# Performance work log

Measured on AMD Instinct MI355X. Metric: run time of the kernel, lower is better.

## Reference

```python
import jax, jax.numpy as jnp
import numpy as np
from jax import lax

# Resolved Optuna hyperparameters
NPOINTS = (512, 256, 128)
RADII = (0.2, 0.4, 0.8)
KS = (32, 32, 32)
BN_EPS = 1e-5


def _fps_single(pts, npoint):
    """Farthest point sampling on one cloud. pts: (N,3) -> (npoint,) int32."""
    N = pts.shape[0]
    def step(carry, _):
        dists, last = carry
        d = jnp.sum((pts - pts[last]) ** 2, axis=-1)
        dists = jnp.minimum(dists, d)
        nxt = jnp.argmax(dists).astype(jnp.int32)
        return (dists, nxt), last
    init = (jnp.full((N,), 1e10, pts.dtype), jnp.int32(0))
    (_, _), idx = lax.scan(step, init, None, length=npoint)
    return idx


def _set_abstraction(xyz, feat, W, b, radius, k, npoint):
    """xyz: (B,N,3), feat: (B,N,C_in) -> new_xyz (B,S,3), new_feat (B,S,C_out)."""
    B, N, _ = xyz.shape
    fps_idx = jax.vmap(lambda p: _fps_single(p, npoint))(xyz)          # (B,S)
    new_xyz = jax.vmap(lambda x, i: x[i])(xyz, fps_idx)                # (B,S,3)
    # ball query: squared distances centers -> all points
    d2 = jnp.sum((new_xyz[:, :, None, :] - xyz[:, None, :, :]) ** 2, axis=-1)  # (B,S,N)
    valid = d2 <= radius * radius
    ar = jnp.arange(N, dtype=jnp.int32)
    gi = jnp.where(valid, ar[None, None, :], N)                        # invalid -> N
    gi = jnp.sort(gi, axis=-1)[:, :, :k]                               # first k in index order
    first = gi[:, :, :1]
    gi = jnp.where(gi == N, first, gi)                                 # pad with first valid (center itself)
    g_xyz = jax.vmap(lambda x, i: x[i])(xyz, gi)                       # (B,S,k,3)
    rel = g_xyz - new_xyz[:, :, None, :]
    g_feat = jax.vmap(lambda x, i: x[i])(feat, gi)                     # (B,S,k,C_in)
    h = jnp.concatenate([rel, g_feat], axis=-1)                        # (B,S,k,3+C_in)
    h = jax.nn.relu(jnp.einsum('bskc,co->bsko', h, W) + b)
    return new_xyz, jnp.max(h, axis=2)                                 # max-pool over group


def _bn(x, g, b):
    # nn.BatchNorm1d training-mode forward (batch statistics, biased var)
    m = x.mean(axis=0)
    v = x.var(axis=0)
    return (x - m) * lax.rsqrt(v + BN_EPS) * g + b


def setup_inputs() -> dict:
    key = jax.random.key(0)
    ks = jax.random.split(key, 8)
    def w(k, i, o):
        return (jax.random.normal(k, (i, o), jnp.float32) / np.sqrt(i)).astype(jnp.float32)
    return dict(
        points=jax.random.uniform(ks[0], (16, 4096, 3), jnp.float32),
        W1=w(ks[1], 3 + 3, 64),   b1=jnp.zeros((64,), jnp.float32),
        W2=w(ks[2], 64 + 3, 128), b2=jnp.zeros((128,), jnp.float32),
        W3=w(ks[3], 128 + 3, 256), b3=jnp.zeros((256,), jnp.float32),
        fc1_w=w(ks[4], 256, 256), fc1_b=jnp.zeros((256,), jnp.float32),
        fc2_w=w(ks[5], 256, 128), fc2_b=jnp.zeros((128,), jnp.float32),
        fc3_w=w(ks[6], 128, 12),  fc3_b=jnp.zeros((12,), jnp.float32),
        bn1_g=jnp.ones((256,), jnp.float32), bn1_b=jnp.zeros((256,), jnp.float32),
        bn2_g=jnp.ones((128,), jnp.float32), bn2_b=jnp.zeros((128,), jnp.float32),
    )


def reference(points, W1, b1, W2, b2, W3, b3, fc1_w, fc1_b, fc2_w, fc2_b,
              fc3_w, fc3_b, bn1_g, bn1_b, bn2_g, bn2_b):
    B = points.shape[0]
    xyz, feat = points, points
    for (W, bb, r, k, s) in ((W1, b1, RADII[0], KS[0], NPOINTS[0]),
                             (W2, b2, RADII[1], KS[1], NPOINTS[1]),
                             (W3, b3, RADII[2], KS[2], NPOINTS[2])):
        xyz, feat = _set_abstraction(xyz, feat, W, bb, r, k, s)
    f = jnp.max(feat, axis=1)                                          # (B, ch3)
    x = jax.nn.relu(_bn(f @ fc1_w + fc1_b, bn1_g, bn1_b))              # dropout: eval-mode identity
    x = jax.nn.relu(_bn(x @ fc2_w + fc2_b, bn2_g, bn2_b))
    x = x @ fc3_w + fc3_b
    return x.reshape(B, 4, 3)
```

## Files before the change

### kernel.cpp

```cpp
#include <hip/hip_runtime.h>
#include <hip/hip_bf16.h>


#define B_SZ 16

template<int CTRL>
__device__ __forceinline__ float dpp_mv(float v) {
    const int i = __float_as_int(v);
    const int r = __builtin_amdgcn_update_dpp(i, i, CTRL, 0xf, 0xf, false);
    return __int_as_float(r);
}

__device__ __forceinline__ float wave_max_f32(float x) {
    float v = x;
    v = fmaxf(v, dpp_mv<0x111>(v));
    v = fmaxf(v, dpp_mv<0x112>(v));
    v = fmaxf(v, dpp_mv<0x114>(v));
    v = fmaxf(v, dpp_mv<0x118>(v));
    v = fmaxf(v, dpp_mv<0x142>(v));
    v = fmaxf(v, dpp_mv<0x143>(v));
    return __uint_as_float(__builtin_amdgcn_readlane(__float_as_uint(v), 63));
}

__device__ __forceinline__ float read_lane_f32(float v, int l) {
    return __uint_as_float(__builtin_amdgcn_readlane(__float_as_uint(v), l));
}

template<int N, int NPOINT, int BLOCK>
__global__ __launch_bounds__(BLOCK) void fps_kernel(
    const float* __restrict__ xyz,
    float* __restrict__ newxyz)
{
    constexpr int P  = N / BLOCK;
    constexpr int NW = BLOCK / 64;
    __shared__ float4 part[2][NW];
    __shared__ float  outb[NPOINT * 3];

    const int b = blockIdx.x, tid = threadIdx.x;
    const int lane = tid & 63, w = tid >> 6;
    const float* xb = xyz + (size_t)b * N * 3;

    float px[P], py[P], pz[P], dd[P];
    const int base = tid * P;
#pragma unroll
    for (int i = 0; i < P; i++) {
        px[i] = xb[(base + i) * 3 + 0];
        py[i] = xb[(base + i) * 3 + 1];
        pz[i] = xb[(base + i) * 3 + 2];
        dd[i] = 1e10f;
    }
    float lx = xb[0], ly = xb[1], lz = xb[2];
    if (tid == 0) { outb[0] = lx; outb[1] = ly; outb[2] = lz; }

    for (int s = 1; s < NPOINT; s++) {
        float bv = -1.0f, bx = 0.0f, by = 0.0f, bz = 0.0f;
#pragma unroll
        for (int i = 0; i < P; i++) {
            const float dx = px[i] - lx, dy = py[i] - ly, dz = pz[i] - lz;
            const float d2 = __fadd_rn(__fadd_rn(__fmul_rn(dx, dx), __fmul_rn(dy, dy)),
                                       __fmul_rn(dz, dz));
            const float nd = fminf(dd[i], d2);
            dd[i] = nd;
            const bool gt = nd > bv;
            bv = gt ? nd : bv;
            bx = gt ? px[i] : bx;
            by = gt ? py[i] : by;
            bz = gt ? pz[i] : bz;
        }
        const float wmax = wave_max_f32(bv);
        const unsigned long long mset = __ballot(bv == wmax);
        const int li = __ffsll(mset) - 1;
        const int buf = s & 1;
        if (lane == li) part[buf][w] = make_float4(bv, bx, by, bz);
        __syncthreads();
        float cv = -1.0f;
#pragma unroll
        for (int q = 0; q < NW; q++) {
            const float4 pq = part[buf][q];
            const bool gt = pq.x > cv;
            cv = gt ? pq.x : cv;
            lx = gt ? pq.y : lx;
            ly = gt ? pq.z : ly;
            lz = gt ? pq.w : lz;
        }
        if (tid == 0) {
            outb[s * 3 + 0] = lx; outb[s * 3 + 1] = ly; outb[s * 3 + 2] = lz;
        }
    }
    __syncthreads();
    float* o = newxyz + (size_t)b * NPOINT * 3;
    for (int t = tid; t < NPOINT * 3; t += BLOCK) o[t] = outb[t];
}

template<int N, int NPOINT>
__device__ __forceinline__ void fps_wave_body(
    const float* __restrict__ xyz,
    float* __restrict__ newxyz,
    const int b, const int lane)
{
    constexpr int P = N / 64;
    const float* xb = xyz + (size_t)b * N * 3;

    float px[P], py[P], pz[P], dd[P];
    const int base = lane * P;
#pragma unroll
    for (int i = 0; i < P; i++) {
        px[i] = xb[(base + i) * 3 + 0];
        py[i] = xb[(base + i) * 3 + 1];
        pz[i] = xb[(base + i) * 3 + 2];
        dd[i] = 1e10f;
    }
#pragma unroll
    for (int i = 0; i < P; i++) {
        asm volatile("" : "+v"(px[i]), "+v"(py[i]), "+v"(pz[i]));
    }
    float lx = xb[0], ly = xb[1], lz = xb[2];
    if (lane == 0) {
        float* o = newxyz + (size_t)b * NPOINT * 3;
        o[0] = lx; o[1] = ly; o[2] = lz;
    }

    for (int s = 1; s < NPOINT; s++) {
        float bv = -1.0f, bx = 0.0f, by = 0.0f, bz = 0.0f;
#pragma unroll
        for (int i = 0; i < P; i++) {
            const float dx = px[i] - lx, dy = py[i] - ly, dz = pz[i] - lz;
            const float d2 = __fadd_rn(__fadd_rn(__fmul_rn(dx, dx), __fmul_rn(dy, dy)),
                                       __fmul_rn(dz, dz));
            const float nd = fminf(dd[i], d2);
            dd[i] = nd;
            const bool gt = nd > bv;
            bv = gt ? nd : bv;
            bx = gt ? px[i] : bx;
            by = gt ? py[i] : by;
            bz = gt ? pz[i] : bz;
        }
        const float wmax = wave_max_f32(bv);
        const unsigned long long mset = __ballot(bv == wmax);
        const int li = __ffsll(mset) - 1;
        lx = read_lane_f32(bx, li);
        ly = read_lane_f32(by, li);
        lz = read_lane_f32(bz, li);
        if (lane == 0) {
            float* o = newxyz + ((size_t)b * NPOINT + s) * 3;
            o[0] = lx; o[1] = ly; o[2] = lz;
        }
    }
}

template<int N, int S, int CF, int COUT, int R>
__device__ __forceinline__ void sa_body(
    const float* __restrict__ xyz,
    const float* __restrict__ feat,
    const float* __restrict__ cent,
    const float* __restrict__ W,
    const float* __restrict__ bias,
    float* __restrict__ outf,
    const float r2, const int s, const int b, const int lane)
{
    constexpr int K    = 32;
    constexpr int JT   = 16;
    constexpr int CIN  = CF + 3;
    constexpr int CINP = (CIN + 3) & ~3;
    constexpr int C4   = CIN & ~3;
    __shared__ int   gi[K];
    __shared__ float h[JT * CINP];

    const float* xb = xyz  + (size_t)b * N * 3;
    const float* fb = feat + (size_t)b * N * CF;
    const float cx = cent[((size_t)b * S + s) * 3 + 0];
    const float cy = cent[((size_t)b * S + s) * 3 + 1];
    const float cz = cent[((size_t)b * S + s) * 3 + 2];

    constexpr int RND = N / 256;
    int total = 0, g0 = 0;
    for (int r0 = 0; r0 < RND; r0++) {
        if (total >= K) break;
        float xs[4], ys[4], zs[4];
#pragma unroll
        for (int c4 = 0; c4 < 4; c4++) {
            const int p = (r0 * 4 + c4) * 64 + lane;
            xs[c4] = xb[p * 3 + 0];
            ys[c4] = xb[p * 3 + 1];
            zs[c4] = xb[p * 3 + 2];
        }
#pragma unroll
        for (int c4 = 0; c4 < 4; c4++) {
            const int p = (r0 * 4 + c4) * 64 + lane;
            const float dx = xs[c4] - cx, dy = ys[c4] - cy, dz = zs[c4] - cz;
            const float d2 = __fadd_rn(__fadd_rn(__fmul_rn(dx, dx), __fmul_rn(dy, dy)),
                                       __fmul_rn(dz, dz));
            const bool v = (d2 <= r2);
            const unsigned long long bal = __ballot(v);
            if (total == 0 && bal != 0ull) g0 = (r0 * 4 + c4) * 64 + (__ffsll(bal) - 1);
            const int pos = total + __popcll(bal & ((1ull << lane) - 1ull));
            if (v && pos < K) gi[pos] = p;
            total += __popcll(bal);
        }
    }
    if (lane == 0 && total < K) {
        for (int q = total; q < K; q++) gi[q] = g0;
    }
    __syncthreads();

    float m[R];
#pragma unroll
    for (int r = 0; r < R; r++) m[r] = -1e30f;

    for (int pass = 0; pass < K / JT; pass++) {
        for (int jj = 0; jj < JT; jj++) {
            const int idx = gi[pass * JT + jj];
            for (int c = lane; c < CIN; c += 64) {
                float val;
                if (c < 3) {
                    const float cc = (c == 0) ? cx : ((c == 1) ? cy : cz);
                    val = xb[idx * 3 + c] - cc;
                } else {
                    val = fb[(size_t)idx * CF + (c - 3)];
                }
                h[jj * CINP + c] = val;
            }
        }
        __syncthreads();

        float acc[JT][R];
#pragma unroll
        for (int jj = 0; jj < JT; jj++)
#pragma unroll
            for (int r = 0; r < R; r++) acc[jj][r] = 0.0f;

        const float* wp = W + lane;
        int c = 0;
        for (; c < C4; c += 4) {
            float wv[4][R];
#pragma unroll
            for (int q = 0; q < 4; q++)
#pragma unroll
                for (int r = 0; r < R; r++)
                    wv[q][r] = wp[(size_t)(c + q) * COUT + r * 64];
#pragma unroll
            for (int jj = 0; jj < JT; jj++) {
                const float4 hv = *(const float4*)&h[jj * CINP + c];
#pragma unroll
                for (int r = 0; r < R; r++) {
                    acc[jj][r] = fmaf(hv.x, wv[0][r], acc[jj][r]);
                    acc[jj][r] = fmaf(hv.y, wv[1][r], acc[jj][r]);
                    acc[jj][r] = fmaf(hv.z, wv[2][r], acc[jj][r]);
                    acc[jj][r] = fmaf(hv.w, wv[3][r], acc[jj][r]);
                }
            }
        }
        for (; c < CIN; c++) {
            float wv[R];
#pragma unroll
            for (int r = 0; r < R; r++) wv[r] = wp[(size_t)c * COUT + r * 64];
#pragma unroll
            for (int jj = 0; jj < JT; jj++) {
                const float hv = h[jj * CINP + c];
#pragma unroll
                for (int r = 0; r < R; r++)
                    acc[jj][r] = fmaf(hv, wv[r], acc[jj][r]);
            }
        }
#pragma unroll
        for (int jj = 0; jj < JT; jj++)
#pragma unroll
            for (int r = 0; r < R; r++) m[r] = fmaxf(m[r], acc[jj][r]);
        __syncthreads();
    }

#pragma unroll
    for (int r = 0; r < R; r++) {
        const int o = r * 64 + lane;
        outf[((size_t)b * S + s) * COUT + o] = fmaxf(bias[o] + m[r], 0.0f);
    }
}

template<int N, int S, int CF, int COUT, int R>
__global__ __launch_bounds__(64) void sa_kernel(
    const float* __restrict__ xyz, const float* __restrict__ feat,
    const float* __restrict__ cent, const float* __restrict__ W,
    const float* __restrict__ bias, float* __restrict__ outf, const float r2)
{
    sa_body<N, S, CF, COUT, R>(xyz, feat, cent, W, bias, outf, r2,
                               blockIdx.x, blockIdx.y, threadIdx.x);
}

template<int NF, int NPF, int N, int S, int CF, int COUT, int R>
__global__ __launch_bounds__(64) void fused_fps_sa_kernel(
    const float* __restrict__ fxyz,
    float* __restrict__ fnew,
    const float* __restrict__ xyz, const float* __restrict__ feat,
    const float* __restrict__ cent, const float* __restrict__ W,
    const float* __restrict__ bias, float* __restrict__ outf, const float r2)
{
    if (blockIdx.x < B_SZ) {
        __builtin_amdgcn_s_setprio(3);
        fps_wave_body<NF, NPF>(fxyz, fnew, blockIdx.x, threadIdx.x);
    } else {
        const int i = blockIdx.x - B_SZ;
        sa_body<N, S, CF, COUT, R>(xyz, feat, cent, W, bias, outf, r2,
                                   i % S, i / S, threadIdx.x);
    }
}

__global__ __launch_bounds__(256) void maxpool_kernel(
    const float* __restrict__ feat,
    float* __restrict__ out)
{
    const int b = blockIdx.x, o = threadIdx.x;
    const float* fb = feat + (size_t)b * 128 * 256 + o;
    float m = fb[0];
#pragma unroll 4
    for (int s1 = 1; s1 < 128; s1++) m = fmaxf(m, fb[(size_t)s1 * 256]);
    out[b * 256 + o] = m;
}

__global__ __launch_bounds__(256) void head_kernel(
    const float* __restrict__ f,
    const float* __restrict__ fc1_w, const float* __restrict__ fc1_b,
    const float* __restrict__ fc2_w, const float* __restrict__ fc2_b,
    const float* __restrict__ fc3_w, const float* __restrict__ fc3_b,
    const float* __restrict__ bn1_g, const float* __restrict__ bn1_b,
    const float* __restrict__ bn2_g, const float* __restrict__ bn2_b,
    float* __restrict__ out)
{
    __shared__ float fl[16 * 257];
    __shared__ float x1[16 * 257];
    __shared__ float x2[16 * 129];
    const int tid = threadIdx.x;

    for (int idx = tid; idx < 16 * 256; idx += 256) {
        const int r = idx >> 8, c = idx & 255;
        fl[r * 257 + c] = f[idx];
    }
    __syncthreads();

    {
        const int r = tid >> 4, g = tid & 15;
        float acc[16];
#pragma unroll
        for (int i = 0; i < 16; i++) acc[i] = fc1_b[g * 16 + i];
        const float* wrow = fc1_w + g * 16;
        for (int c = 0; c < 256; c++) {
            const float fv = fl[r * 257 + c];
            const float4* w4 = (const float4*)(wrow + (size_t)c * 256);
#pragma unroll
            for (int q = 0; q < 4; q++) {
                const float4 wv = w4[q];
                acc[q * 4 + 0] = fmaf(fv, wv.x, acc[q * 4 + 0]);
                acc[q * 4 + 1] = fmaf(fv, wv.y, acc[q * 4 + 1]);
                acc[q * 4 + 2] = fmaf(fv, wv.z, acc[q * 4 + 2]);
                acc[q * 4 + 3] = fmaf(fv, wv.w, acc[q * 4 + 3]);
            }
        }
#pragma unroll
        for (int i = 0; i < 16; i++) x1[r * 257 + g * 16 + i] = acc[i];
    }
    __syncthreads();
    {
        const int o = tid;
        float v[16];
#pragma unroll
        for (int r = 0; r < 16; r++) v[r] = x1[r * 257 + o];
        float m = 0.0f;
#pragma unroll
        for (int r = 0; r < 16; r++) m += v[r];
        m *= (1.0f / 16.0f);
        float var = 0.0f;
#pragma unroll
        for (int r = 0; r < 16; r++) { const float d = v[r] - m; var += d * d; }
        var *= (1.0f / 16.0f);
        const float sc = bn1_g[o] / sqrtf(var + 1e-5f);
        const float sh = bn1_b[o];
#pragma unroll
        for (int r = 0; r < 16; r++)
            x1[r * 257 + o] = fmaxf((v[r] - m) * sc + sh, 0.0f);
    }
    __syncthreads();
    {
        const int r = tid >> 4, g = tid & 15;
        float acc[8];
#pragma unroll
        for (int i = 0; i < 8; i++) acc[i] = fc2_b[g * 8 + i];
        const float* wrow = fc2_w + g * 8;
        for (int c = 0; c < 256; c++) {
            const float fv = x1[r * 257 + c];
            const float4* w4 = (const float4*)(wrow + (size_t)c * 128);
#pragma unroll
            for (int q = 0; q < 2; q++) {
                const float4 wv = w4[q];
                acc[q * 4 + 0] = fmaf(fv, wv.x, acc[q * 4 + 0]);
                acc[q * 4 + 1] = fmaf(fv, wv.y, acc[q * 4 + 1]);
                acc[q * 4 + 2] = fmaf(fv, wv.z, acc[q * 4 + 2]);
                acc[q * 4 + 3] = fmaf(fv, wv.w, acc[q * 4 + 3]);
            }
        }
#pragma unroll
        for (int i = 0; i < 8; i++) x2[r * 129 + g * 8 + i] = acc[i];
    }
    __syncthreads();
    if (tid < 128) {
        const int o = tid;
        float v[16];
#pragma unroll
        for (int r = 0; r < 16; r++) v[r] = x2[r * 129 + o];
        float m = 0.0f;
#pragma unroll
        for (int r = 0; r < 16; r++) m += v[r];
        m *= (1.0f / 16.0f);
        float var = 0.0f;
#pragma unroll
        for (int r = 0; r < 16; r++) { const float d = v[r] - m; var += d * d; }
        var *= (1.0f / 16.0f);
        const float sc = bn2_g[o] / sqrtf(var + 1e-5f);
        const float sh = bn2_b[o];
#pragma unroll
        for (int r = 0; r < 16; r++)
            x2[r * 129 + o] = fmaxf((v[r] - m) * sc + sh, 0.0f);
    }
    __syncthreads();
    if (tid < 192) {
        const int r = tid / 12, j = tid - r * 12;
        float acc = fc3_b[j];
        for (int c = 0; c < 128; c++)
            acc = fmaf(x2[r * 129 + c], fc3_w[c * 12 + j], acc);
        out[r * 12 + j] = acc;
    }
}

extern "C" void kernel_launch(void* const* d_in, const int* in_sizes, int n_in,
                              void* d_out, int out_size, void* d_ws, size_t ws_size,
                              hipStream_t stream) {
    const float* points = (const float*)d_in[0];
    const float* W1     = (const float*)d_in[1];
    const float* b1     = (const float*)d_in[2];
    const float* W2     = (const float*)d_in[3];
    const float* b2     = (const float*)d_in[4];
    const float* W3     = (const float*)d_in[5];
    const float* b3     = (const float*)d_in[6];
    const float* fc1_w  = (const float*)d_in[7];
    const float* fc1_b  = (const float*)d_in[8];
    const float* fc2_w  = (const float*)d_in[9];
    const float* fc2_b  = (const float*)d_in[10];
    const float* fc3_w  = (const float*)d_in[11];
    const float* fc3_b  = (const float*)d_in[12];
    const float* bn1_g  = (const float*)d_in[13];
    const float* bn1_b  = (const float*)d_in[14];
    const float* bn2_g  = (const float*)d_in[15];
    const float* bn2_b  = (const float*)d_in[16];
    float* out = (float*)d_out;

    float* ws   = (float*)d_ws;
    float* nx1  = ws;
    float* f1   = nx1 + 24576;
    float* nx2  = f1  + 524288;
    float* f2   = nx2 + 12288;
    float* nx3  = f2  + 524288;
    float* f3   = nx3 + 6144;
    float* fmx  = f3  + 524288;

    fps_kernel<4096, 512, 512><<<B_SZ, 512, 0, stream>>>(points, nx1);
    fused_fps_sa_kernel<512, 256, 4096, 512, 3, 64, 1>
        <<<B_SZ + 512 * B_SZ, 64, 0, stream>>>(
        nx1, nx2, points, points, nx1, W1, b1, f1, (float)(0.2 * 0.2));
    fused_fps_sa_kernel<256, 128, 512, 256, 64, 128, 2>
        <<<B_SZ + 256 * B_SZ, 64, 0, stream>>>(
        nx2, nx3, nx1, f1, nx2, W2, b2, f2, (float)(0.4 * 0.4));
    sa_kernel<256, 128, 128, 256, 4><<<dim3(128, B_SZ), 64, 0, stream>>>(
        nx2, f2, nx3, W3, b3, f3, (float)(0.8 * 0.8));
    maxpool_kernel<<<B_SZ, 256, 0, stream>>>(f3, fmx);
    head_kernel<<<1, 256, 0, stream>>>(fmx, fc1_w, fc1_b, fc2_w, fc2_b,
                                       fc3_w, fc3_b, bn1_g, bn1_b, bn2_g, bn2_b,
                                       out);
}
```

Baseline: 799.2 us.

## Split first FPS into two launches, fuse SA3 maxpool via atomics, parallelize fc1

```diff
diff --git a/kernel.cpp b/kernel.cpp
--- a/kernel.cpp
+++ b/kernel.cpp
@@ -26,15 +26,17 @@
     return __uint_as_float(__builtin_amdgcn_readlane(__float_as_uint(v), l));
 }
 
-template<int N, int NPOINT, int BLOCK>
+template<int N, int NPOINT, int BLOCK, int S0, int S1, bool FIRST>
 __global__ __launch_bounds__(BLOCK) void fps_kernel(
     const float* __restrict__ xyz,
-    float* __restrict__ newxyz)
+    float* __restrict__ newxyz,
+    float* __restrict__ dstate)
 {
     constexpr int P  = N / BLOCK;
     constexpr int NW = BLOCK / 64;
+    constexpr int O0 = FIRST ? 0 : S0;
     __shared__ float4 part[2][NW];
-    __shared__ float  outb[NPOINT * 3];
+    __shared__ float  outb[(S1 - O0) * 3];
 
     const int b = blockIdx.x, tid = threadIdx.x;
     const int lane = tid & 63, w = tid >> 6;
@@ -47,12 +49,21 @@
         px[i] = xb[(base + i) * 3 + 0];
         py[i] = xb[(base + i) * 3 + 1];
         pz[i] = xb[(base + i) * 3 + 2];
-        dd[i] = 1e10f;
-    }
-    float lx = xb[0], ly = xb[1], lz = xb[2];
-    if (tid == 0) { outb[0] = lx; outb[1] = ly; outb[2] = lz; }
-
-    for (int s = 1; s < NPOINT; s++) {
+    }
+    float lx, ly, lz;
+    if (FIRST) {
+#pragma unroll
+        for (int i = 0; i < P; i++) dd[i] = 1e10f;
+        lx = xb[0]; ly = xb[1]; lz = xb[2];
+        if (tid == 0) { outb[0] = lx; outb[1] = ly; outb[2] = lz; }
+    } else {
+#pragma unroll
+        for (int i = 0; i < P; i++) dd[i] = dstate[((size_t)b * P + i) * BLOCK + tid];
+        const float* c = newxyz + ((size_t)b * NPOINT + (S0 - 1)) * 3;
+        lx = c[0]; ly = c[1]; lz = c[2];
+    }
+
+    for (int s = S0; s < S1; s++) {
         float bv = -1.0f, bx = 0.0f, by = 0.0f, bz = 0.0f;
 #pragma unroll
         for (int i = 0; i < P; i++) {
@@ -84,12 +95,18 @@
             lz = gt ? pq.w : lz;
         }
         if (tid == 0) {
-            outb[s * 3 + 0] = lx; outb[s * 3 + 1] = ly; outb[s * 3 + 2] = lz;
-        }
-    }
-    __syncthreads();
-    float* o = newxyz + (size_t)b * NPOINT * 3;
-    for (int t = tid; t < NPOINT * 3; t += BLOCK) o[t] = outb[t];
+            const int t = (s - O0) * 3;
+            outb[t + 0] = lx; outb[t + 1] = ly; outb[t + 2] = lz;
+        }
+    }
+    __syncthreads();
+    if (S1 < NPOINT) {
+#pragma unroll
+        for (int i = 0; i < P; i++)
+            dstate[((size_t)b * P + i) * BLOCK + tid] = dd[i];
+    }
+    float* o = newxyz + ((size_t)b * NPOINT + O0) * 3;
+    for (int t = tid; t < (S1 - O0) * 3; t += BLOCK) o[t] = outb[t];
 }
 
 template<int N, int NPOINT>
@@ -148,7 +165,7 @@
     }
 }
 
-template<int N, int S, int CF, int COUT, int R>
+template<int N, int S, int CF, int COUT, int R, bool AMAX>
 __device__ __forceinline__ void sa_body(
     const float* __restrict__ xyz,
     const float* __restrict__ feat,
@@ -272,18 +289,23 @@
 #pragma unroll
     for (int r = 0; r < R; r++) {
         const int o = r * 64 + lane;
-        outf[((size_t)b * S + s) * COUT + o] = fmaxf(bias[o] + m[r], 0.0f);
-    }
-}
-
-template<int N, int S, int CF, int COUT, int R>
+        const float val = fmaxf(bias[o] + m[r], 0.0f);
+        if (AMAX) {
+            atomicMax((unsigned*)&outf[(size_t)b * COUT + o], __float_as_uint(val));
+        } else {
+            outf[((size_t)b * S + s) * COUT + o] = val;
+        }
+    }
+}
+
+template<int N, int S, int CF, int COUT, int R, bool AMAX>
 __global__ __launch_bounds__(64) void sa_kernel(
     const float* __restrict__ xyz, const float* __restrict__ feat,
     const float* __restrict__ cent, const float* __restrict__ W,
     const float* __restrict__ bias, float* __restrict__ outf, const float r2)
 {
-    sa_body<N, S, CF, COUT, R>(xyz, feat, cent, W, bias, outf, r2,
-                               blockIdx.x, blockIdx.y, threadIdx.x);
+    sa_body<N, S, CF, COUT, R, AMAX>(xyz, feat, cent, W, bias, outf, r2,
+                                     blockIdx.x, blockIdx.y, threadIdx.x);
 }
 
 template<int NF, int NPF, int N, int S, int CF, int COUT, int R>
@@ -299,63 +321,45 @@
         fps_wave_body<NF, NPF>(fxyz, fnew, blockIdx.x, threadIdx.x);
     } else {
         const int i = blockIdx.x - B_SZ;
-        sa_body<N, S, CF, COUT, R>(xyz, feat, cent, W, bias, outf, r2,
-                                   i % S, i / S, threadIdx.x);
-    }
-}
-
-__global__ __launch_bounds__(256) void maxpool_kernel(
-    const float* __restrict__ feat,
-    float* __restrict__ out)
-{
-    const int b = blockIdx.x, o = threadIdx.x;
-    const float* fb = feat + (size_t)b * 128 * 256 + o;
-    float m = fb[0];
-#pragma unroll 4
-    for (int s1 = 1; s1 < 128; s1++) m = fmaxf(m, fb[(size_t)s1 * 256]);
-    out[b * 256 + o] = m;
-}
-
-__global__ __launch_bounds__(256) void head_kernel(
+        sa_body<N, S, CF, COUT, R, false>(xyz, feat, cent, W, bias, outf, r2,
+                                          i % S, i / S, threadIdx.x);
+    }
+}
+
+__global__ __launch_bounds__(64) void fc1_kernel(
     const float* __restrict__ f,
-    const float* __restrict__ fc1_w, const float* __restrict__ fc1_b,
+    const float* __restrict__ w,
+    const float* __restrict__ bias,
+    float* __restrict__ x1h)
+{
+    const int r = blockIdx.x >> 2;
+    const int o = (blockIdx.x & 3) * 64 + threadIdx.x;
+    const float* fr = f + r * 256;
+    float acc = bias[o];
+    for (int c = 0; c < 256; c += 4) {
+        acc = fmaf(fr[c + 0], w[(size_t)(c + 0) * 256 + o], acc);
+        acc = fmaf(fr[c + 1], w[(size_t)(c + 1) * 256 + o], acc);
+        acc = fmaf(fr[c + 2], w[(size_t)(c + 2) * 256 + o], acc);
+        acc = fmaf(fr[c + 3], w[(size_t)(c + 3) * 256 + o], acc);
+    }
+    x1h[r * 256 + o] = acc;
+}
+
+__global__ __launch_bounds__(256) void head2_kernel(
+    const float* __restrict__ x1h,
     const float* __restrict__ fc2_w, const float* __restrict__ fc2_b,
     const float* __restrict__ fc3_w, const float* __restrict__ fc3_b,
     const float* __restrict__ bn1_g, const float* __restrict__ bn1_b,
     const float* __restrict__ bn2_g, const float* __restrict__ bn2_b,
     float* __restrict__ out)
 {
-    __shared__ float fl[16 * 257];
     __shared__ float x1[16 * 257];
     __shared__ float x2[16 * 129];
     const int tid = threadIdx.x;
 
     for (int idx = tid; idx < 16 * 256; idx += 256) {
         const int r = idx >> 8, c = idx & 255;
-        fl[r * 257 + c] = f[idx];
-    }
-    __syncthreads();
-
-    {
-        const int r = tid >> 4, g = tid & 15;
-        float acc[16];
-#pragma unroll
-        for (int i = 0; i < 16; i++) acc[i] = fc1_b[g * 16 + i];
-        const float* wrow = fc1_w + g * 16;
-        for (int c = 0; c < 256; c++) {
-            const float fv = fl[r * 257 + c];
-            const float4* w4 = (const float4*)(wrow + (size_t)c * 256);
-#pragma unroll
-            for (int q = 0; q < 4; q++) {
-                const float4 wv = w4[q];
-                acc[q * 4 + 0] = fmaf(fv, wv.x, acc[q * 4 + 0]);
-                acc[q * 4 + 1] = fmaf(fv, wv.y, acc[q * 4 + 1]);
-                acc[q * 4 + 2] = fmaf(fv, wv.z, acc[q * 4 + 2]);
-                acc[q * 4 + 3] = fmaf(fv, wv.w, acc[q * 4 + 3]);
-            }
-        }
-#pragma unroll
-        for (int i = 0; i < 16; i++) x1[r * 257 + g * 16 + i] = acc[i];
+        x1[r * 257 + c] = x1h[idx];
     }
     __syncthreads();
     {
@@ -457,20 +461,24 @@
     float* nx2  = f1  + 524288;
     float* f2   = nx2 + 12288;
     float* nx3  = f2  + 524288;
-    float* f3   = nx3 + 6144;
-    float* fmx  = f3  + 524288;
-
-    fps_kernel<4096, 512, 512><<<B_SZ, 512, 0, stream>>>(points, nx1);
+    float* fmx  = nx3 + 6144;
+    float* fdd  = fmx + 4096;
+    float* x1h  = fdd + 65536;
+
+    fps_kernel<4096, 512, 512, 1, 256, true><<<B_SZ, 512, 0, stream>>>(
+        points, nx1, fdd);
+    fps_kernel<4096, 512, 512, 256, 512, false><<<B_SZ, 512, 0, stream>>>(
+        points, nx1, fdd);
     fused_fps_sa_kernel<512, 256, 4096, 512, 3, 64, 1>
         <<<B_SZ + 512 * B_SZ, 64, 0, stream>>>(
         nx1, nx2, points, points, nx1, W1, b1, f1, (float)(0.2 * 0.2));
     fused_fps_sa_kernel<256, 128, 512, 256, 64, 128, 2>
         <<<B_SZ + 256 * B_SZ, 64, 0, stream>>>(
         nx2, nx3, nx1, f1, nx2, W2, b2, f2, (float)(0.4 * 0.4));
-    sa_kernel<256, 128, 128, 256, 4><<<dim3(128, B_SZ), 64, 0, stream>>>(
-        nx2, f2, nx3, W3, b3, f3, (float)(0.8 * 0.8));
-    maxpool_kernel<<<B_SZ, 256, 0, stream>>>(f3, fmx);
-    head_kernel<<<1, 256, 0, stream>>>(fmx, fc1_w, fc1_b, fc2_w, fc2_b,
-                                       fc3_w, fc3_b, bn1_g, bn1_b, bn2_g, bn2_b,
-                                       out);
-}
+    hipMemsetAsync(fmx, 0, 16 * 256 * sizeof(float), stream);
+    sa_kernel<256, 128, 128, 256, 4, true><<<dim3(128, B_SZ), 64, 0, stream>>>(
+        nx2, f2, nx3, W3, b3, fmx, (float)(0.8 * 0.8));
+    fc1_kernel<<<64, 64, 0, stream>>>(fmx, fc1_w, fc1_b, x1h);
+    head2_kernel<<<1, 256, 0, stream>>>(x1h, fc2_w, fc2_b, fc3_w, fc3_b,
+                                        bn1_g, bn1_b, bn2_g, bn2_b, out);
+}
```

New measurement: 717.2 us. -10.3%, faster.
